# Optimization experiments

Measured on AMD Instinct MI355X. Metric: run time of the kernel, lower is better.

The kernel has to match this reference:

```python
import jax, jax.numpy as jnp
import numpy as np

N_NEIGHBORS = 5
N_TRAIN = 65536
N_TEST = 4096
DIM = 512
N_CLASSES = 10


def setup_inputs() -> dict:
    key = jax.random.key(0)
    k1, k2, k3 = jax.random.split(key, 3)
    X_train = jax.random.normal(k1, (N_TRAIN, DIM), dtype=jnp.float32)
    X_test = jax.random.normal(k2, (N_TEST, DIM), dtype=jnp.float32)
    y_train = jax.random.randint(k3, (N_TRAIN,), 0, N_CLASSES, dtype=jnp.int64)
    return {"X_train": X_train, "X_test": X_test, "y_train": y_train}


def _knn_predict(X_train, X_test, y_train, k):
    # Euclidean distances via the expanded form (GEMM-dominated):
    # ||t - x||^2 = ||t||^2 + ||x||^2 - 2 t.x
    t2 = jnp.sum(X_test * X_test, axis=-1, keepdims=True)          # [Nt, 1]
    x2 = jnp.sum(X_train * X_train, axis=-1)                        # [Ntr]
    cross = X_test @ X_train.T                                      # [Nt, Ntr]
    d2 = jnp.maximum(t2 + x2[None, :] - 2.0 * cross, 0.0)
    distances = jnp.sqrt(d2)                                        # cdist p=2

    # k smallest distances -> neighbor indices
    _, indices = jax.lax.top_k(-distances, k)                       # [Nt, k]
    nearest = y_train[indices]                                      # [Nt, k]

    counts = jnp.sum(nearest[:, :, None] == nearest[:, None, :], axis=-1)  # [Nt,k,k]->[Nt,k]
    max_c = jnp.max(counts, axis=-1, keepdims=True)
    big = jnp.iinfo(nearest.dtype).max
    candidates = jnp.where(counts == max_c, nearest, big)
    predictions = jnp.min(candidates, axis=-1)                      # [Nt]
    return predictions


def reference(X_train, X_test, y_train):
    return _knn_predict(X_train, X_test, y_train, N_NEIGHBORS)
```

## Files before the change

### kernel.cpp

```cpp
#include <hip/hip_runtime.h>
#include <cstdint>

#define N_TRAIN 65536
#define N_TEST  4096
#define DIM     512
#define K_NN    5
#define NSEG    32
#define SEG     (N_TRAIN / NSEG)

#define BTM 128
#define BTN 256
#define GBK 128
#define NCAND (NSEG * K_NN)
#define NRES  24
#define NSTEP ((SEG / BTN) * (DIM / GBK))
#define KMASK 0xFFFFF800u

typedef float f32x4  __attribute__((ext_vector_type(4)));
typedef float f32x16 __attribute__((ext_vector_type(16)));
typedef int   i32x8  __attribute__((ext_vector_type(8)));

#define GLDS16(g, l)                                                          \
    __builtin_amdgcn_global_load_lds(                                         \
        (__attribute__((address_space(1))) void*)(g),                         \
        (__attribute__((address_space(3))) void*)(l), 16, 0, 0)

__device__ inline unsigned f2e4m3_sw(float x) {
    float ax = fabsf(x);
    unsigned sgn = (__float_as_uint(x) >> 31) << 7;
    if (ax != ax) return sgn | 0x7Fu;
    if (ax >= 448.0f) return sgn | 0x7Eu;
    int ebits = (int)((__float_as_uint(ax) >> 23) & 0xFF);
    int e = ebits - 127;
    int shift = (e < -6 ? -6 : e) - 3;
    float q = exp2f((float)shift);
    float r = rintf(ax / q) * q;
    if (r >= 448.0f) return sgn | 0x7Eu;
    if (r == 0.0f) return sgn;
    unsigned ru = __float_as_uint(r);
    int re = (int)((ru >> 23) & 0xFF) - 127;
    if (re < -6) {
        unsigned k = (unsigned)(r * 512.0f);
        return sgn | k;
    }
    unsigned rm = (ru >> 20) & 0x7u;
    return sgn | ((unsigned)(re + 7) << 3) | rm;
}

__device__ inline unsigned pk4_fp8(float x0, float x1, float x2, float x3) {
#if __has_builtin(__builtin_amdgcn_cvt_pk_fp8_f32)
    unsigned r = (unsigned)__builtin_amdgcn_cvt_pk_fp8_f32(x0, x1, 0, 0);
    r = (unsigned)__builtin_amdgcn_cvt_pk_fp8_f32(x2, x3, (int)r, 1);
    return r;
#else
    return f2e4m3_sw(x0) | (f2e4m3_sw(x1) << 8) |
           (f2e4m3_sw(x2) << 16) | (f2e4m3_sw(x3) << 24);
#endif
}

__global__ __launch_bounds__(256) void cvtnorm8_k(const float* __restrict__ in,
                                                  unsigned char* __restrict__ outb,
                                                  float* __restrict__ outn,
                                                  int nrows) {
    int row  = blockIdx.x * 4 + (threadIdx.x >> 6);
    int lane = threadIdx.x & 63;
    if (row >= nrows) return;
    const float4* p = (const float4*)(in + (size_t)row * DIM) + lane * 2;
    float4 a = p[0], b = p[1];
    float s = a.x*a.x + a.y*a.y + a.z*a.z + a.w*a.w
            + b.x*b.x + b.y*b.y + b.z*b.z + b.w*b.w;
    uint2 v;
    v.x = pk4_fp8(a.x, a.y, a.z, a.w);
    v.y = pk4_fp8(b.x, b.y, b.z, b.w);
    *((uint2*)(outb + (size_t)row * DIM) + lane) = v;
#pragma unroll
    for (int off = 32; off > 0; off >>= 1) s += __shfl_xor(s, off, 64);
    if (lane == 0) outn[row] = s;
}

__global__ __launch_bounds__(256) void norms_k(const float* __restrict__ X,
                                               float* __restrict__ out,
                                               int nrows) {
    int row  = blockIdx.x * 4 + (threadIdx.x >> 6);
    int lane = threadIdx.x & 63;
    if (row >= nrows) return;
    const float4* xp = (const float4*)(X + (size_t)row * DIM);
    float4 a = xp[lane];
    float4 b = xp[lane + 64];
    float s = a.x*a.x + a.y*a.y + a.z*a.z + a.w*a.w
            + b.x*b.x + b.y*b.y + b.z*b.z + b.w*b.w;
#pragma unroll
    for (int off = 32; off > 0; off >>= 1) s += __shfl_down(s, off, 64);
    if (lane == 0) out[row] = s;
}

__device__ inline void ins5(unsigned long long key, unsigned long long* top) {
    if (key < top[4]) {
        unsigned long long k0 = top[0], k1 = top[1], k2 = top[2], k3 = top[3];
        top[0] = key < k0 ? key : k0;
        top[1] = key < k0 ? k0 : (key < k1 ? key : k1);
        top[2] = key < k1 ? k1 : (key < k2 ? key : k2);
        top[3] = key < k2 ? k2 : (key < k3 ? key : k3);
        top[4] = key < k3 ? k3 : key;
    }
}

__device__ inline void ins5u(unsigned key, unsigned* top) {
    if (key < top[4]) {
        unsigned k0 = top[0], k1 = top[1], k2 = top[2], k3 = top[3];
        top[0] = key < k0 ? key : k0;
        top[1] = key < k0 ? k0 : (key < k1 ? key : k1);
        top[2] = key < k1 ? k1 : (key < k2 ? key : k2);
        top[3] = key < k2 ? k2 : (key < k3 ? key : k3);
        top[4] = key < k3 ? k3 : key;
    }
}

__device__ inline unsigned fmono(float v) {
    unsigned u = __float_as_uint(v);
    return (u & 0x80000000u) ? ~u : (u | 0x80000000u);
}

__global__ __launch_bounds__(512, 1) void knn_mfma_k(
    const unsigned char* __restrict__ Xtr8,
    const unsigned char* __restrict__ Xte8,
    const float* __restrict__ x2,
    unsigned* __restrict__ cand)
{
    __shared__ __align__(16) unsigned char As[4][BTM * GBK];
    __shared__ __align__(16) unsigned char Bs[2][BTN * GBK];

    const int t    = threadIdx.x;
    const int lane = t & 63;
    const int w    = t >> 6;
    const int wr   = w >> 1, wc = w & 1;
    const int l31  = lane & 31;
    const int hi   = lane >> 5;
    const int fz   = (((l31 & 7) ^ ((l31 >> 3) & 3)) << 4);
    const int row0 = blockIdx.x * BTM;
    const int seg0 = blockIdx.y * SEG;

    unsigned top5[2][K_NN];
#pragma unroll
    for (int nt = 0; nt < 2; ++nt)
#pragma unroll
        for (int p = 0; p < K_NN; ++p) top5[nt][p] = 0xFFFFFFFFu;

#pragma unroll
    for (int j = 0; j < 8; ++j) {
        const int c  = j * 512 + t;
        const int rw = (c >> 3) & 127;
        const int f3 = (rw & 7) ^ ((rw >> 3) & 3);
        GLDS16(Xte8 + (size_t)(row0 + rw) * DIM + (c >> 10) * GBK
                    + (((c & 7) ^ f3) << 4),
               &As[0][0] + (j * 512 + w * 64) * 16);
    }

    int offB[4];
#pragma unroll
    for (int j = 0; j < 4; ++j) {
        const int cs = j * 512 + t;
        const int gr = cs >> 3;
        const int f3 = (gr & 7) ^ ((gr >> 3) & 3);
        offB[j] = gr * DIM + (((cs ^ f3) & 7) << 4);
    }

    auto stageB = [&](int s, int b) {
        const unsigned char* bb =
            Xtr8 + (size_t)(seg0 + (s >> 2) * BTN) * DIM + (s & 3) * GBK;
#pragma unroll
        for (int j = 0; j < 4; ++j)
            GLDS16(bb + offB[j], &Bs[b][0] + (j * 512 + w * 64) * 16);
    };

    f32x16 acc[2][2];
    auto zero_acc = [&]() {
#pragma unroll
        for (int mt = 0; mt < 2; ++mt)
#pragma unroll
            for (int nt = 0; nt < 2; ++nt)
#pragma unroll
                for (int e = 0; e < 16; ++e) acc[mt][nt][e] = 0.f;
    };

    auto epilogue = [&](int ct) {
        const int col0 = seg0 + ct * BTN;
        f32x4 x2r[2][4];
#pragma unroll
        for (int mt = 0; mt < 2; ++mt)
#pragma unroll
            for (int g = 0; g < 4; ++g)
                x2r[mt][g] = *(const f32x4*)&x2[col0 + wr * 64 + mt * 32 + g * 8 + 4 * hi];
        const int cbase = ct * BTN + wr * 64;
#pragma unroll
        for (int nt = 0; nt < 2; ++nt) {
            float dv[2][16];
            float gm[2][4];
#pragma unroll
            for (int mt = 0; mt < 2; ++mt)
#pragma unroll
                for (int g = 0; g < 4; ++g) {
#pragma unroll
                    for (int i = 0; i < 4; ++i)
                        dv[mt][g * 4 + i] =
                            fmaf(-2.f, acc[mt][nt][g * 4 + i], x2r[mt][g][i]);
                    gm[mt][g] = fminf(fminf(dv[mt][g*4+0], dv[mt][g*4+1]),
                                      fminf(dv[mt][g*4+2], dv[mt][g*4+3]));
                }
            float dmin = fminf(
                fminf(fminf(gm[0][0], gm[0][1]), fminf(gm[0][2], gm[0][3])),
                fminf(fminf(gm[1][0], gm[1][1]), fminf(gm[1][2], gm[1][3])));
            if ((fmono(dmin) & KMASK) <= top5[nt][4]) {
#pragma unroll
                for (int mt = 0; mt < 2; ++mt)
#pragma unroll
                    for (int g = 0; g < 4; ++g) {
                        if ((fmono(gm[mt][g]) & KMASK) <= top5[nt][4]) {
#pragma unroll
                            for (int i = 0; i < 4; ++i) {
                                unsigned key = (fmono(dv[mt][g * 4 + i]) & KMASK)
                                    | (unsigned)(cbase + mt * 32 + g * 8 + 4 * hi + i);
                                ins5u(key, top5[nt]);
                            }
                        }
                    }
            }
        }
    };

    stageB(0, 0);
    __syncthreads();

    zero_acc();

#pragma unroll 1
    for (int s = 0; s < NSTEP; ++s) {
        if (s + 1 < NSTEP) stageB(s + 1, (s + 1) & 1);

        const unsigned char* Ab = As[s & 3];
        const unsigned char* Bb = Bs[s & 1];
#pragma unroll
        for (int ks = 0; ks < 2; ++ks) {
            const int xq = (ks * 64 + hi * 32) ^ fz;
            i32x8 trf[2], tef[2];
#pragma unroll
            for (int mt = 0; mt < 2; ++mt) {
                const unsigned char* p = &Bb[(wr * 64 + mt * 32 + l31) * GBK];
                int4 lo = *(const int4*)&p[xq];
                int4 hx = *(const int4*)&p[xq ^ 16];
                trf[mt] = (i32x8){lo.x, lo.y, lo.z, lo.w, hx.x, hx.y, hx.z, hx.w};
            }
#pragma unroll
            for (int nt = 0; nt < 2; ++nt) {
                const unsigned char* p = &Ab[(wc * 64 + nt * 32 + l31) * GBK];
                int4 lo = *(const int4*)&p[xq];
                int4 hx = *(const int4*)&p[xq ^ 16];
                tef[nt] = (i32x8){lo.x, lo.y, lo.z, lo.w, hx.x, hx.y, hx.z, hx.w};
            }
#pragma unroll
            for (int mt = 0; mt < 2; ++mt)
#pragma unroll
                for (int nt = 0; nt < 2; ++nt)
                    acc[mt][nt] = __builtin_amdgcn_mfma_scale_f32_32x32x64_f8f6f4(
                        trf[mt], tef[nt], acc[mt][nt],
                        0 , 0 ,
                        0, 0x7F7F7F7F, 0, 0x7F7F7F7F );
        }

        __syncthreads();

        if ((s & 3) == 3) {
            epilogue(s >> 2);
            zero_acc();
        }
    }

    __syncthreads();
    unsigned* MB = (unsigned*)&As[0][0];
#pragma unroll
    for (int nt = 0; nt < 2; ++nt)
#pragma unroll
        for (int p = 0; p < K_NN; ++p) MB[t * 10 + nt * K_NN + p] = top5[nt][p];
    __syncthreads();

    if (t < BTM) {
        const int r   = t;
        const int mwc = r >> 6, mnt = (r >> 5) & 1, mn5 = r & 31;
        unsigned tp[K_NN];
#pragma unroll
        for (int p = 0; p < K_NN; ++p) tp[p] = 0xFFFFFFFFu;
#pragma unroll
        for (int w2 = 0; w2 < 4; ++w2)
#pragma unroll
            for (int h2 = 0; h2 < 2; ++h2) {
                const int tid = (w2 * 2 + mwc) * 64 + h2 * 32 + mn5;
                const unsigned* src = &MB[tid * 10 + mnt * K_NN];
#pragma unroll
                for (int p = 0; p < K_NN; ++p) ins5u(src[p], tp);
            }
        unsigned* cr = cand + (size_t)(row0 + r) * NCAND + blockIdx.y * K_NN;
#pragma unroll
        for (int p = 0; p < K_NN; ++p) cr[p] = tp[p];
    }
}

__global__ __launch_bounds__(256) void rescore_vote_k(
    const float* __restrict__ Xtr, const float* __restrict__ Xte,
    const float* __restrict__ x2,  const float* __restrict__ t2,
    const unsigned* __restrict__ cand,
    const int* __restrict__ y, int* __restrict__ out)
{
    int row  = blockIdx.x * 4 + (threadIdx.x >> 6);
    int lane = threadIdx.x & 63;
    const unsigned* cr = cand + (size_t)row * NCAND;

    auto expand = [](unsigned k, int e) -> unsigned long long {
        unsigned gcol = (unsigned)(e / K_NN) * SEG + (k & 0x7FFu);
        return ((unsigned long long)k << 32) | gcol;
    };
    unsigned long long c0 = expand(cr[lane], lane);
    unsigned long long c1 = expand(cr[64 + lane], 64 + lane);
    unsigned long long c2 = (lane < NCAND - 128)
                          ? expand(cr[128 + lane], 128 + lane) : ~0ull;

    unsigned cols[NRES];
#pragma unroll 1
    for (int i = 0; i < NRES; ++i) {
        unsigned long long m = c0 < c1 ? c0 : c1;
        m = c2 < m ? c2 : m;
#pragma unroll
        for (int off = 32; off > 0; off >>= 1) {
            unsigned long long o = __shfl_xor(m, off, 64);
            m = o < m ? o : m;
        }
        cols[i] = (unsigned)(m & 0xffffffffu);
        if (c0 == m) c0 = ~0ull;
        if (c1 == m) c1 = ~0ull;
        if (c2 == m) c2 = ~0ull;
    }

    const float4* te = (const float4*)(Xte + (size_t)row * DIM);
    float4 e0 = te[lane * 2], e1 = te[lane * 2 + 1];
    float t2r = t2[row];
    float d2s[NRES];
#pragma unroll 4
    for (int i = 0; i < NRES; ++i) {
        const float4* tr = (const float4*)(Xtr + (size_t)cols[i] * DIM);
        float4 p = tr[lane * 2], q = tr[lane * 2 + 1];
        float s = e0.x * p.x;
        s = fmaf(e0.y, p.y, s); s = fmaf(e0.z, p.z, s); s = fmaf(e0.w, p.w, s);
        s = fmaf(e1.x, q.x, s); s = fmaf(e1.y, q.y, s);
        s = fmaf(e1.z, q.z, s); s = fmaf(e1.w, q.w, s);
#pragma unroll
        for (int off = 32; off > 0; off >>= 1) s += __shfl_xor(s, off, 64);
        d2s[i] = fmaxf(t2r + x2[cols[i]] - 2.0f * s, 0.0f);
    }

    unsigned long long top[K_NN];
#pragma unroll
    for (int p = 0; p < K_NN; ++p) top[p] = ~0ull;
#pragma unroll
    for (int i = 0; i < NRES; ++i)
        ins5(((unsigned long long)__float_as_uint(d2s[i]) << 32) | cols[i], top);

    if (lane == 0) {
        int labs[K_NN];
#pragma unroll
        for (int p = 0; p < K_NN; ++p) labs[p] = y[(unsigned)(top[p] & 0xffffffffu)];
        int bestLab = 0x7fffffff, bestCnt = 0;
#pragma unroll
        for (int p = 0; p < K_NN; ++p) {
            int cnt = 0;
#pragma unroll
            for (int q = 0; q < K_NN; ++q) cnt += (labs[q] == labs[p]) ? 1 : 0;
            if (cnt > bestCnt || (cnt == bestCnt && labs[p] < bestLab)) {
                bestCnt = cnt; bestLab = labs[p];
            }
        }
        out[row] = bestLab;
    }
}

#define FTM 64
#define FTN 128
#define FBK 16
#define FSEG (N_TRAIN / 8)

__global__ __launch_bounds__(256) void knn_tile_k(
    const float* __restrict__ Xtr, const float* __restrict__ Xte,
    const float* __restrict__ x2,  const float* __restrict__ t2,
    unsigned long long* __restrict__ cand)
{
    __shared__ float As[FBK][FTM];
    __shared__ float Bs[FBK][FTN];
    __shared__ unsigned long long MB[FTM][16 * K_NN];

    const int t   = threadIdx.x;
    const int ty  = t >> 4;
    const int tx  = t & 15;
    const int row0 = blockIdx.x * FTM;
    const int seg0 = blockIdx.y * FSEG;

    float t2r[4];
#pragma unroll
    for (int j = 0; j < 4; ++j) t2r[j] = t2[row0 + ty * 4 + j];

    unsigned long long top[4][K_NN];
#pragma unroll
    for (int j = 0; j < 4; ++j)
#pragma unroll
        for (int p = 0; p < K_NN; ++p) top[j][p] = ~0ull;

    const int srow = t >> 2;
    const int skq  = (t & 3) * 4;

    for (int ct = 0; ct < FSEG / FTN; ++ct) {
        const int col0 = seg0 + ct * FTN;
        float acc[4][8] = {};

        for (int k0 = 0; k0 < DIM; k0 += FBK) {
            float4 av  = *(const float4*)(Xte + (size_t)(row0 + srow) * DIM + k0 + skq);
            float4 bv0 = *(const float4*)(Xtr + (size_t)(col0 + srow) * DIM + k0 + skq);
            float4 bv1 = *(const float4*)(Xtr + (size_t)(col0 + 64 + srow) * DIM + k0 + skq);
            __syncthreads();
            As[skq + 0][srow] = av.x;  As[skq + 1][srow] = av.y;
            As[skq + 2][srow] = av.z;  As[skq + 3][srow] = av.w;
            Bs[skq + 0][srow] = bv0.x; Bs[skq + 1][srow] = bv0.y;
            Bs[skq + 2][srow] = bv0.z; Bs[skq + 3][srow] = bv0.w;
            Bs[skq + 0][srow + 64] = bv1.x; Bs[skq + 1][srow + 64] = bv1.y;
            Bs[skq + 2][srow + 64] = bv1.z; Bs[skq + 3][srow + 64] = bv1.w;
            __syncthreads();

#pragma unroll
            for (int k = 0; k < FBK; ++k) {
                float4 a  = *(const float4*)&As[k][ty * 4];
                float4 b0 = *(const float4*)&Bs[k][tx * 8];
                float4 b1 = *(const float4*)&Bs[k][tx * 8 + 4];
                float a4[4] = {a.x, a.y, a.z, a.w};
                float b8[8] = {b0.x, b0.y, b0.z, b0.w, b1.x, b1.y, b1.z, b1.w};
#pragma unroll
                for (int j = 0; j < 4; ++j)
#pragma unroll
                    for (int l = 0; l < 8; ++l)
                        acc[j][l] = fmaf(a4[j], b8[l], acc[j][l]);
            }
        }

#pragma unroll
        for (int j = 0; j < 4; ++j) {
#pragma unroll
            for (int l = 0; l < 8; ++l) {
                int col = col0 + tx * 8 + l;
                float d2 = fmaxf(t2r[j] + x2[col] - 2.0f * acc[j][l], 0.0f);
                unsigned long long key =
                    ((unsigned long long)__float_as_uint(d2) << 32) | (unsigned)col;
                ins5(key, top[j]);
            }
        }
    }

#pragma unroll
    for (int j = 0; j < 4; ++j)
#pragma unroll
        for (int p = 0; p < K_NN; ++p)
            MB[ty * 4 + j][tx * K_NN + p] = top[j][p];
    __syncthreads();

    if (t < FTM) {
        unsigned long long last = 0;
        for (int p = 0; p < K_NN; ++p) {
            unsigned long long best = ~0ull;
            for (int q = 0; q < 16 * K_NN; ++q) {
                unsigned long long v = MB[t][q];
                if (v > last && v < best) best = v;
            }
            cand[(size_t)(row0 + t) * 40 + blockIdx.y * K_NN + p] = best;
            last = best;
        }
    }
}

__global__ __launch_bounds__(256) void knn_final_k(
    const unsigned long long* __restrict__ cand,
    const int* __restrict__ y, int* __restrict__ out)
{
    int r = blockIdx.x * 256 + threadIdx.x;
    if (r >= N_TEST) return;
    const unsigned long long* c = cand + (size_t)r * 40;

    unsigned long long top[K_NN];
#pragma unroll
    for (int p = 0; p < K_NN; ++p) top[p] = ~0ull;
#pragma unroll
    for (int i = 0; i < 40; ++i) ins5(c[i], top);

    int labs[K_NN];
#pragma unroll
    for (int p = 0; p < K_NN; ++p) labs[p] = y[(unsigned)(top[p] & 0xffffffffu)];

    int bestLab = 0x7fffffff, bestCnt = 0;
#pragma unroll
    for (int p = 0; p < K_NN; ++p) {
        int cnt = 0;
#pragma unroll
        for (int q = 0; q < K_NN; ++q) cnt += (labs[q] == labs[p]) ? 1 : 0;
        if (cnt > bestCnt || (cnt == bestCnt && labs[p] < bestLab)) {
            bestCnt = cnt; bestLab = labs[p];
        }
    }
    out[r] = bestLab;
}

extern "C" void kernel_launch(void* const* d_in, const int* in_sizes, int n_in,
                              void* d_out, int out_size, void* d_ws, size_t ws_size,
                              hipStream_t stream) {
    const float* Xtr = (const float*)d_in[0];
    const float* Xte = (const float*)d_in[1];
    const int*   y   = (const int*)d_in[2];
    int* out = (int*)d_out;

    char* ws = (char*)d_ws;
    float* x2 = (float*)ws;
    float* t2 = (float*)(ws + 262144);

    const size_t NEED = 74448896;

    if (ws_size >= NEED) {
        unsigned* cand = (unsigned*)(ws + 278528);
        unsigned char* Xte8 = (unsigned char*)(ws + 3145728);
        unsigned char* Xtr8 = (unsigned char*)(ws + 7340032);

        cvtnorm8_k<<<N_TRAIN / 4, 256, 0, stream>>>(Xtr, Xtr8, x2, N_TRAIN);
        cvtnorm8_k<<<N_TEST / 4, 256, 0, stream>>>(Xte, Xte8, t2, N_TEST);

        knn_mfma_k<<<dim3(N_TEST / BTM, NSEG), 512, 0, stream>>>(Xtr8, Xte8, x2, cand);
        rescore_vote_k<<<N_TEST / 4, 256, 0, stream>>>(Xtr, Xte, x2, t2, cand, y, out);
    } else {
        unsigned long long* cand = (unsigned long long*)(ws + 278528);
        norms_k<<<N_TRAIN / 4, 256, 0, stream>>>(Xtr, x2, N_TRAIN);
        norms_k<<<N_TEST / 4, 256, 0, stream>>>(Xte, t2, N_TEST);
        knn_tile_k<<<dim3(N_TEST / FTM, 8), 256, 0, stream>>>(Xtr, Xte, x2, t2, cand);
        knn_final_k<<<N_TEST / 256, 256, 0, stream>>>(cand, y, out);
    }
}
```

Baseline: 552.3 us.

## Halve train tile width and stream test tile per step for higher occupancy

Shrinks the train tile from 256 to 128 columns and stops keeping the whole test tile resident in LDS. The test slice is now double-buffered and restaged each k-step alongside the train slice. LDS and accumulator registers drop, and launch bounds now request 4 blocks per CU so more waves can hide latency. The cost is reloading the test tile for every column tile and doing fewer MFMAs per LDS fragment load.

Result: faster. 481.7 us (-12.8%).

```diff
diff --git a/kernel.cpp b/kernel.cpp
--- a/kernel.cpp
+++ b/kernel.cpp
@@ -9,7 +9,7 @@
 #define SEG     (N_TRAIN / NSEG)
 
 #define BTM 128
-#define BTN 256
+#define BTN 128
 #define GBK 128
 #define NCAND (NSEG * K_NN)
 #define NRES  24
@@ -121,13 +121,13 @@
     return (u & 0x80000000u) ? ~u : (u | 0x80000000u);
 }
 
-__global__ __launch_bounds__(512, 1) void knn_mfma_k(
+__global__ __launch_bounds__(512, 4) void knn_mfma_k(
     const unsigned char* __restrict__ Xtr8,
     const unsigned char* __restrict__ Xte8,
     const float* __restrict__ x2,
     unsigned* __restrict__ cand)
 {
-    __shared__ __align__(16) unsigned char As[4][BTM * GBK];
+    __shared__ __align__(16) unsigned char As[2][BTM * GBK];
     __shared__ __align__(16) unsigned char Bs[2][BTN * GBK];
 
     const int t    = threadIdx.x;
@@ -146,109 +146,92 @@
 #pragma unroll
         for (int p = 0; p < K_NN; ++p) top5[nt][p] = 0xFFFFFFFFu;
 
-#pragma unroll
-    for (int j = 0; j < 8; ++j) {
-        const int c  = j * 512 + t;
-        const int rw = (c >> 3) & 127;
-        const int f3 = (rw & 7) ^ ((rw >> 3) & 3);
-        GLDS16(Xte8 + (size_t)(row0 + rw) * DIM + (c >> 10) * GBK
-                    + (((c & 7) ^ f3) << 4),
-               &As[0][0] + (j * 512 + w * 64) * 16);
-    }
-
-    int offB[4];
-#pragma unroll
-    for (int j = 0; j < 4; ++j) {
+    int off[2];
+#pragma unroll
+    for (int j = 0; j < 2; ++j) {
         const int cs = j * 512 + t;
         const int gr = cs >> 3;
         const int f3 = (gr & 7) ^ ((gr >> 3) & 3);
-        offB[j] = gr * DIM + (((cs ^ f3) & 7) << 4);
-    }
-
-    auto stageB = [&](int s, int b) {
+        off[j] = gr * DIM + (((cs ^ f3) & 7) << 4);
+    }
+
+    auto stage = [&](int s, int b) {
+        const int k0 = (s & 3) * GBK;
+        const unsigned char* ab = Xte8 + (size_t)row0 * DIM + k0;
         const unsigned char* bb =
-            Xtr8 + (size_t)(seg0 + (s >> 2) * BTN) * DIM + (s & 3) * GBK;
-#pragma unroll
-        for (int j = 0; j < 4; ++j)
-            GLDS16(bb + offB[j], &Bs[b][0] + (j * 512 + w * 64) * 16);
+            Xtr8 + (size_t)(seg0 + (s >> 2) * BTN) * DIM + k0;
+#pragma unroll
+        for (int j = 0; j < 2; ++j) {
+            const int ldsb = (j * 512 + w * 64) * 16;
+            GLDS16(ab + off[j], &As[b][ldsb]);
+            GLDS16(bb + off[j], &Bs[b][ldsb]);
+        }
     };
 
-    f32x16 acc[2][2];
+    f32x16 acc[2];
     auto zero_acc = [&]() {
 #pragma unroll
-        for (int mt = 0; mt < 2; ++mt)
-#pragma unroll
-            for (int nt = 0; nt < 2; ++nt)
-#pragma unroll
-                for (int e = 0; e < 16; ++e) acc[mt][nt][e] = 0.f;
+        for (int nt = 0; nt < 2; ++nt)
+#pragma unroll
+            for (int e = 0; e < 16; ++e) acc[nt][e] = 0.f;
     };
 
     auto epilogue = [&](int ct) {
         const int col0 = seg0 + ct * BTN;
-        f32x4 x2r[2][4];
-#pragma unroll
-        for (int mt = 0; mt < 2; ++mt)
-#pragma unroll
-            for (int g = 0; g < 4; ++g)
-                x2r[mt][g] = *(const f32x4*)&x2[col0 + wr * 64 + mt * 32 + g * 8 + 4 * hi];
-        const int cbase = ct * BTN + wr * 64;
+        f32x4 x2r[4];
+#pragma unroll
+        for (int g = 0; g < 4; ++g)
+            x2r[g] = *(const f32x4*)&x2[col0 + wr * 32 + g * 8 + 4 * hi];
+        const int cbase = ct * BTN + wr * 32;
 #pragma unroll
         for (int nt = 0; nt < 2; ++nt) {
-            float dv[2][16];
-            float gm[2][4];
-#pragma unroll
-            for (int mt = 0; mt < 2; ++mt)
+            float dv[16];
+            float gm[4];
+#pragma unroll
+            for (int g = 0; g < 4; ++g) {
+#pragma unroll
+                for (int i = 0; i < 4; ++i)
+                    dv[g * 4 + i] = fmaf(-2.f, acc[nt][g * 4 + i], x2r[g][i]);
+                gm[g] = fminf(fminf(dv[g*4+0], dv[g*4+1]),
+                              fminf(dv[g*4+2], dv[g*4+3]));
+            }
+            float dmin = fminf(fminf(gm[0], gm[1]), fminf(gm[2], gm[3]));
+            if ((fmono(dmin) & KMASK) <= top5[nt][4]) {
 #pragma unroll
                 for (int g = 0; g < 4; ++g) {
-#pragma unroll
-                    for (int i = 0; i < 4; ++i)
-                        dv[mt][g * 4 + i] =
-                            fmaf(-2.f, acc[mt][nt][g * 4 + i], x2r[mt][g][i]);
-                    gm[mt][g] = fminf(fminf(dv[mt][g*4+0], dv[mt][g*4+1]),
-                                      fminf(dv[mt][g*4+2], dv[mt][g*4+3]));
-                }
-            float dmin = fminf(
-                fminf(fminf(gm[0][0], gm[0][1]), fminf(gm[0][2], gm[0][3])),
-                fminf(fminf(gm[1][0], gm[1][1]), fminf(gm[1][2], gm[1][3])));
-            if ((fmono(dmin) & KMASK) <= top5[nt][4]) {
-#pragma unroll
-                for (int mt = 0; mt < 2; ++mt)
-#pragma unroll
-                    for (int g = 0; g < 4; ++g) {
-                        if ((fmono(gm[mt][g]) & KMASK) <= top5[nt][4]) {
-#pragma unroll
-                            for (int i = 0; i < 4; ++i) {
-                                unsigned key = (fmono(dv[mt][g * 4 + i]) & KMASK)
-                                    | (unsigned)(cbase + mt * 32 + g * 8 + 4 * hi + i);
-                                ins5u(key, top5[nt]);
-                            }
+                    if ((fmono(gm[g]) & KMASK) <= top5[nt][4]) {
+#pragma unroll
+                        for (int i = 0; i < 4; ++i) {
+                            unsigned key = (fmono(dv[g * 4 + i]) & KMASK)
+                                | (unsigned)(cbase + g * 8 + 4 * hi + i);
+                            ins5u(key, top5[nt]);
                         }
                     }
+                }
             }
         }
     };
 
-    stageB(0, 0);
+    stage(0, 0);
     __syncthreads();
 
     zero_acc();
 
 #pragma unroll 1
     for (int s = 0; s < NSTEP; ++s) {
-        if (s + 1 < NSTEP) stageB(s + 1, (s + 1) & 1);
-
-        const unsigned char* Ab = As[s & 3];
+        if (s + 1 < NSTEP) stage(s + 1, (s + 1) & 1);
+
+        const unsigned char* Ab = As[s & 1];
         const unsigned char* Bb = Bs[s & 1];
 #pragma unroll
         for (int ks = 0; ks < 2; ++ks) {
             const int xq = (ks * 64 + hi * 32) ^ fz;
-            i32x8 trf[2], tef[2];
-#pragma unroll
-            for (int mt = 0; mt < 2; ++mt) {
-                const unsigned char* p = &Bb[(wr * 64 + mt * 32 + l31) * GBK];
+            i32x8 trf, tef[2];
+            {
+                const unsigned char* p = &Bb[(wr * 32 + l31) * GBK];
                 int4 lo = *(const int4*)&p[xq];
                 int4 hx = *(const int4*)&p[xq ^ 16];
-                trf[mt] = (i32x8){lo.x, lo.y, lo.z, lo.w, hx.x, hx.y, hx.z, hx.w};
+                trf = (i32x8){lo.x, lo.y, lo.z, lo.w, hx.x, hx.y, hx.z, hx.w};
             }
 #pragma unroll
             for (int nt = 0; nt < 2; ++nt) {
@@ -258,13 +241,11 @@
                 tef[nt] = (i32x8){lo.x, lo.y, lo.z, lo.w, hx.x, hx.y, hx.z, hx.w};
             }
 #pragma unroll
-            for (int mt = 0; mt < 2; ++mt)
-#pragma unroll
-                for (int nt = 0; nt < 2; ++nt)
-                    acc[mt][nt] = __builtin_amdgcn_mfma_scale_f32_32x32x64_f8f6f4(
-                        trf[mt], tef[nt], acc[mt][nt],
-                        0 , 0 ,
-                        0, 0x7F7F7F7F, 0, 0x7F7F7F7F );
+            for (int nt = 0; nt < 2; ++nt)
+                acc[nt] = __builtin_amdgcn_mfma_scale_f32_32x32x64_f8f6f4(
+                    trf, tef[nt], acc[nt],
+                    0 , 0 ,
+                    0, 0x7F7F7F7F, 0, 0x7F7F7F7F );
         }
 
         __syncthreads();
```
